# Optimization experiments

Hardware: AMD Instinct MI355X
Metric: run time of the kernel (lower is better)

The kernel has to match this reference:

```python
import jax, jax.numpy as jnp
import numpy as np

B, D, M, NKEYS = 2048, 128, 256, 32768
EST_CONST = np.float32(np.sqrt(np.pi / 2.0) / M)  # sqrt(pi/2)/projection_dim


def setup_inputs() -> dict:
    key = jax.random.key(0)
    k1, k2, k3, k4 = jax.random.split(key, 4)
    query = jax.random.normal(k1, (B, D), dtype=jnp.float32)
    # cached keys are sign-quantized JL sketches (+/-1), as produced by quantize_keys
    cached_keys = jnp.sign(jax.random.normal(k2, (NKEYS, M), dtype=jnp.float32))
    # norms of the original keys: positive, realistic magnitude ~ sqrt(D)
    key_norms = jax.random.uniform(k3, (NKEYS,), dtype=jnp.float32, minval=0.5, maxval=1.5) * np.float32(np.sqrt(D))
    sketch_matrix = jax.random.normal(k4, (M, D), dtype=jnp.float32)
    return {"query": query, "cached_keys": cached_keys, "key_norms": key_norms, "sketch_matrix": sketch_matrix}


def reference(query, cached_keys, key_norms, sketch_matrix):
    # projected_query: [B, M]
    projected_query = jnp.einsum('bd,md->bm', query, sketch_matrix)
    # inner products with quantized keys: [B, NKEYS]
    inner_products = jnp.einsum('bm,nm->bn', projected_query, cached_keys)
    estimated_scores = EST_CONST * key_norms * inner_products  # broadcast over n_keys
    return jax.nn.softmax(estimated_scores, axis=-1)
```

## Files before the change

kernel.cpp:

```cpp
#include <hip/hip_runtime.h>


#define NB 2048
#define DD 128
#define MM 256
#define NK 32768
#define EST_CONST 4.8957583489668673e-03f

typedef _Float16 half8 __attribute__((ext_vector_type(8)));
typedef _Float16 half4v __attribute__((ext_vector_type(4)));
typedef float floatx4 __attribute__((ext_vector_type(4)));

__device__ __forceinline__ void async16(const void* g, void* l) {
    __builtin_amdgcn_global_load_lds(
        (const __attribute__((address_space(1))) unsigned int*)g,
        (__attribute__((address_space(3))) unsigned int*)l,
        16, 0, 0);
}

__global__ void proj_kernel(const float* __restrict__ query,
                            const float* __restrict__ sketch,
                            _Float16* __restrict__ proj) {
    __shared__ float q[DD];
    const int b = blockIdx.x;
    const int t = threadIdx.x;
    if (t < DD) q[t] = query[b * DD + t];
    __syncthreads();
    const float* srow = sketch + t * DD;
    float acc = 0.f;
#pragma unroll
    for (int d = 0; d < DD; d += 4) {
        float4 s4 = *(const float4*)(srow + d);
        acc += s4.x * q[d] + s4.y * q[d + 1] + s4.z * q[d + 2] + s4.w * q[d + 3];
    }
    proj[b * MM + t] = (_Float16)acc;
}

__global__ void cvt_keys(const float* __restrict__ keys, _Float16* __restrict__ kh) {
    const int i = blockIdx.x * 256 + threadIdx.x;
    float4 v = ((const float4*)keys)[i];
    half4v h;
    h.x = (_Float16)v.x; h.y = (_Float16)v.y; h.z = (_Float16)v.z; h.w = (_Float16)v.w;
    ((half4v*)kh)[i] = h;
}

__global__ __launch_bounds__(256, 3)
void score_kernel(const _Float16* __restrict__ proj,
                  const _Float16* __restrict__ kh,
                  const float* __restrict__ key_norms,
                  _Float16* __restrict__ scores,
                  float* __restrict__ stats_max,
                  float* __restrict__ stats_sum) {
    __shared__ __align__(16) _Float16 sQ[128 * 64];
    __shared__ __align__(16) _Float16 sK[128 * 64];
    __shared__ float red[128][2];
    __shared__ float redS[128][2];

    const int tid  = threadIdx.x;
    const int lane = tid & 63;
    const int wave = tid >> 6;
    const int quad = lane >> 4;
    const int lc   = lane & 15;
    const int wb   = wave >> 1;
    const int wn   = wave & 1;
    const int rowBase = blockIdx.x * 128;
    const int cb      = blockIdx.y;
    const int colBase = cb * 128;

    floatx4 acc[4][4];
#pragma unroll
    for (int i = 0; i < 4; i++)
#pragma unroll
        for (int j = 0; j < 4; j++) acc[i][j] = (floatx4){0.f, 0.f, 0.f, 0.f};

    const _Float16* gQ[4];
    const _Float16* gK[4];
    int ldsOff[4];
#pragma unroll
    for (int p = 0; p < 4; p++) {
        const int c = p * 256 + tid;
        const int row = c >> 3;
        const int seg = (c & 7) ^ (row & 7);
        gQ[p] = proj + (rowBase + row) * MM + seg * 8;
        gK[p] = kh + (colBase + row) * MM + seg * 8;
        ldsOff[p] = c * 8;
    }

    for (int k0 = 0; k0 < MM; k0 += 64) {
        __syncthreads();
#pragma unroll
        for (int p = 0; p < 4; p++) {
            async16(gQ[p] + k0, &sQ[ldsOff[p]]);
            async16(gK[p] + k0, &sK[ldsOff[p]]);
        }
        __syncthreads();
#pragma unroll
        for (int kk = 0; kk < 2; kk++) {
            const int segSel = ((kk * 4 + quad) ^ (lc & 7)) * 8;
            half8 kf[4], qf[4];
#pragma unroll
            for (int s = 0; s < 4; s++) {
                kf[s] = *(const half8*)&sK[(wn * 64 + s * 16 + lc) * 64 + segSel];
                qf[s] = *(const half8*)&sQ[(wb * 64 + s * 16 + lc) * 64 + segSel];
            }
#pragma unroll
            for (int ib = 0; ib < 4; ib++)
#pragma unroll
                for (int in = 0; in < 4; in++)
                    acc[ib][in] = __builtin_amdgcn_mfma_f32_16x16x32_f16(
                        kf[in], qf[ib], acc[ib][in], 0, 0, 0);
        }
    }

#pragma unroll
    for (int in = 0; in < 4; in++) {
        const float4 nrm = *(const float4*)&key_norms[colBase + wn * 64 + in * 16 + quad * 4];
#pragma unroll
        for (int ib = 0; ib < 4; ib++) {
            acc[ib][in][0] *= EST_CONST * nrm.x;
            acc[ib][in][1] *= EST_CONST * nrm.y;
            acc[ib][in][2] *= EST_CONST * nrm.z;
            acc[ib][in][3] *= EST_CONST * nrm.w;
        }
    }

    float mcb[4];
#pragma unroll
    for (int ib = 0; ib < 4; ib++) {
        float mx = -1e30f;
#pragma unroll
        for (int in = 0; in < 4; in++)
#pragma unroll
            for (int r = 0; r < 4; r++) mx = fmaxf(mx, acc[ib][in][r]);
        mx = fmaxf(mx, __shfl_xor(mx, 16, 64));
        mx = fmaxf(mx, __shfl_xor(mx, 32, 64));
        if (quad == 0) red[wb * 64 + ib * 16 + lc][wn] = mx;
    }
    __syncthreads();
#pragma unroll
    for (int ib = 0; ib < 4; ib++) {
        const int rl = wb * 64 + ib * 16 + lc;
        mcb[ib] = fmaxf(red[rl][0], red[rl][1]);
    }
#pragma unroll
    for (int ib = 0; ib < 4; ib++) {
        float sm = 0.f;
#pragma unroll
        for (int in = 0; in < 4; in++)
#pragma unroll
            for (int r = 0; r < 4; r++) {
                const float e = __expf(acc[ib][in][r] - mcb[ib]);
                acc[ib][in][r] = e;
                sm += e;
            }
        sm += __shfl_xor(sm, 16, 64);
        sm += __shfl_xor(sm, 32, 64);
        if (quad == 0) redS[wb * 64 + ib * 16 + lc][wn] = sm;
    }
#pragma unroll
    for (int ib = 0; ib < 4; ib++) {
        const size_t rowOff = (size_t)(rowBase + wb * 64 + ib * 16 + lc) * NK;
#pragma unroll
        for (int in = 0; in < 4; in++) {
            half4v h;
            h.x = (_Float16)acc[ib][in][0];
            h.y = (_Float16)acc[ib][in][1];
            h.z = (_Float16)acc[ib][in][2];
            h.w = (_Float16)acc[ib][in][3];
            *(half4v*)&scores[rowOff + colBase + wn * 64 + in * 16 + quad * 4] = h;
        }
    }
    __syncthreads();
    if (wn == 0 && quad == 0) {
#pragma unroll
        for (int ib = 0; ib < 4; ib++) {
            const int rl = wb * 64 + ib * 16 + lc;
            const int grow = rowBase + rl;
            stats_max[grow * 256 + cb] = mcb[ib];
            stats_sum[grow * 256 + cb] = redS[rl][0] + redS[rl][1];
        }
    }
}

__global__ void combine_stats(const float* __restrict__ smax, const float* __restrict__ ssum,
                              float* __restrict__ rowM, float* __restrict__ rowR) {
    const int lane = threadIdx.x & 63;
    const int row = blockIdx.x * 4 + (threadIdx.x >> 6);
    const float4 mv = ((const float4*)(smax + row * 256))[lane];
    float m = fmaxf(fmaxf(mv.x, mv.y), fmaxf(mv.z, mv.w));
#pragma unroll
    for (int d = 1; d < 64; d <<= 1) m = fmaxf(m, __shfl_xor(m, d, 64));
    const float4 sv = ((const float4*)(ssum + row * 256))[lane];
    float l = sv.x * __expf(mv.x - m) + sv.y * __expf(mv.y - m) +
              sv.z * __expf(mv.z - m) + sv.w * __expf(mv.w - m);
#pragma unroll
    for (int d = 1; d < 64; d <<= 1) l += __shfl_xor(l, d, 64);
    if (lane == 0) {
        rowM[row] = m;
        rowR[row] = 1.0f / l;
    }
}

__global__ __launch_bounds__(256)
void norm_kernel(const _Float16* __restrict__ scores,
                 const float* __restrict__ smax,
                 const float* __restrict__ rowM, const float* __restrict__ rowR,
                 float* __restrict__ out) {
    const int idx = blockIdx.x * 256 + threadIdx.x;
    const int row = idx >> 12;
    const int c8 = (idx & 4095) << 3;
    const float scale = __expf(smax[row * 256 + (c8 >> 7)] - rowM[row]) * rowR[row];
    const half8 s = *(const half8*)(scores + ((size_t)row << 15) + c8);
    float4 o0, o1;
    o0.x = (float)s[0] * scale; o0.y = (float)s[1] * scale;
    o0.z = (float)s[2] * scale; o0.w = (float)s[3] * scale;
    o1.x = (float)s[4] * scale; o1.y = (float)s[5] * scale;
    o1.z = (float)s[6] * scale; o1.w = (float)s[7] * scale;
    float4* op = (float4*)(out + ((size_t)row << 15) + c8);
    op[0] = o0;
    op[1] = o1;
}

extern "C" void kernel_launch(void* const* d_in, const int* in_sizes, int n_in,
                              void* d_out, int out_size, void* d_ws, size_t ws_size,
                              hipStream_t stream) {
    const float* query  = (const float*)d_in[0];
    const float* keys   = (const float*)d_in[1];
    const float* norms  = (const float*)d_in[2];
    const float* sketch = (const float*)d_in[3];
    float* out = (float*)d_out;

    char* ws = (char*)d_ws;
    const size_t MB = 1024 * 1024;
    _Float16* kh     = (_Float16*)(ws);
    _Float16* proj   = (_Float16*)(ws + 16 * MB);
    _Float16* scores = (_Float16*)(ws + 17 * MB);
    float* smax      = (float*)(ws + 145 * MB);
    float* ssum      = (float*)(ws + 147 * MB);
    float* rowM      = (float*)(ws + 149 * MB);
    float* rowR      = (float*)(ws + 149 * MB + 8192);

    hipLaunchKernelGGL(proj_kernel, dim3(NB), dim3(256), 0, stream, query, sketch, proj);
    hipLaunchKernelGGL(cvt_keys, dim3(NK * MM / 4 / 256), dim3(256), 0, stream, keys, kh);
    hipLaunchKernelGGL(score_kernel, dim3(NB / 128, NK / 128), dim3(256), 0, stream,
                       proj, kh, norms, scores, smax, ssum);
    hipLaunchKernelGGL(combine_stats, dim3(NB / 4), dim3(256), 0, stream,
                       smax, ssum, rowM, rowR);
    hipLaunchKernelGGL(norm_kernel, dim3((NB * NK / 8) / 256), dim3(256), 0, stream,
                       scores, smax, rowM, rowR, out);
}
```

Baseline: 436.3 us.

## Stage score tiles through LDS for coalesced stores and precompute block scales

The score kernel now writes its exp tiles into a padded shared-memory buffer that reuses the Q/K staging space. It then emits full 128-column rows with 16-byte coalesced stores, replacing the scattered 8-byte stores. The grid is transposed so that consecutive blocks walk key columns. combine_stats now precomputes a per-row, per-column-block scale, so norm_kernel does one lookup instead of an exp, and norm_kernel uses 4-wide nontemporal stores. Costs are an extra LDS round trip and barrier, plus more threads in norm_kernel.

```diff
diff --git a/kernel.cpp b/kernel.cpp
--- a/kernel.cpp
+++ b/kernel.cpp
@@ -51,10 +51,11 @@
                   _Float16* __restrict__ scores,
                   float* __restrict__ stats_max,
                   float* __restrict__ stats_sum) {
-    __shared__ __align__(16) _Float16 sQ[128 * 64];
-    __shared__ __align__(16) _Float16 sK[128 * 64];
+    __shared__ __align__(16) _Float16 smem[17408];
     __shared__ float red[128][2];
     __shared__ float redS[128][2];
+    _Float16* sQ = smem;
+    _Float16* sK = smem + 8192;
 
     const int tid  = threadIdx.x;
     const int lane = tid & 63;
@@ -63,9 +64,9 @@
     const int lc   = lane & 15;
     const int wb   = wave >> 1;
     const int wn   = wave & 1;
-    const int rowBase = blockIdx.x * 128;
-    const int cb      = blockIdx.y;
+    const int cb      = blockIdx.x;
     const int colBase = cb * 128;
+    const int rowBase = blockIdx.y * 128;
 
     floatx4 acc[4][4];
 #pragma unroll
@@ -124,7 +125,6 @@
         }
     }
 
-    float mcb[4];
 #pragma unroll
     for (int ib = 0; ib < 4; ib++) {
         float mx = -1e30f;
@@ -137,6 +137,7 @@
         if (quad == 0) red[wb * 64 + ib * 16 + lc][wn] = mx;
     }
     __syncthreads();
+    float mcb[4];
 #pragma unroll
     for (int ib = 0; ib < 4; ib++) {
         const int rl = wb * 64 + ib * 16 + lc;
@@ -146,29 +147,19 @@
     for (int ib = 0; ib < 4; ib++) {
         float sm = 0.f;
 #pragma unroll
-        for (int in = 0; in < 4; in++)
+        for (int in = 0; in < 4; in++) {
+            half4v h;
 #pragma unroll
             for (int r = 0; r < 4; r++) {
                 const float e = __expf(acc[ib][in][r] - mcb[ib]);
-                acc[ib][in][r] = e;
+                h[r] = (_Float16)e;
                 sm += e;
             }
+            *(half4v*)&smem[(wb * 64 + ib * 16 + lc) * 136 + wn * 64 + in * 16 + quad * 4] = h;
+        }
         sm += __shfl_xor(sm, 16, 64);
         sm += __shfl_xor(sm, 32, 64);
         if (quad == 0) redS[wb * 64 + ib * 16 + lc][wn] = sm;
-    }
-#pragma unroll
-    for (int ib = 0; ib < 4; ib++) {
-        const size_t rowOff = (size_t)(rowBase + wb * 64 + ib * 16 + lc) * NK;
-#pragma unroll
-        for (int in = 0; in < 4; in++) {
-            half4v h;
-            h.x = (_Float16)acc[ib][in][0];
-            h.y = (_Float16)acc[ib][in][1];
-            h.z = (_Float16)acc[ib][in][2];
-            h.w = (_Float16)acc[ib][in][3];
-            *(half4v*)&scores[rowOff + colBase + wn * 64 + in * 16 + quad * 4] = h;
-        }
     }
     __syncthreads();
     if (wn == 0 && quad == 0) {
@@ -180,10 +171,18 @@
             stats_sum[grow * 256 + cb] = redS[rl][0] + redS[rl][1];
         }
     }
+#pragma unroll
+    for (int p = 0; p < 8; p++) {
+        const int flat = p * 2048 + tid * 8;
+        const int row = flat >> 7;
+        const int col = flat & 127;
+        half8 v = *(const half8*)&smem[row * 136 + col];
+        *(half8*)&scores[(size_t)(rowBase + row) * NK + colBase + col] = v;
+    }
 }
 
 __global__ void combine_stats(const float* __restrict__ smax, const float* __restrict__ ssum,
-                              float* __restrict__ rowM, float* __restrict__ rowR) {
+                              float* __restrict__ cbscale) {
     const int lane = threadIdx.x & 63;
     const int row = blockIdx.x * 4 + (threadIdx.x >> 6);
     const float4 mv = ((const float4*)(smax + row * 256))[lane];
@@ -195,30 +194,30 @@
               sv.z * __expf(mv.z - m) + sv.w * __expf(mv.w - m);
 #pragma unroll
     for (int d = 1; d < 64; d <<= 1) l += __shfl_xor(l, d, 64);
-    if (lane == 0) {
-        rowM[row] = m;
-        rowR[row] = 1.0f / l;
-    }
+    const float rL = 1.0f / l;
+    float4 sc;
+    sc.x = __expf(mv.x - m) * rL;
+    sc.y = __expf(mv.y - m) * rL;
+    sc.z = __expf(mv.z - m) * rL;
+    sc.w = __expf(mv.w - m) * rL;
+    ((float4*)(cbscale + row * 256))[lane] = sc;
 }
 
 __global__ __launch_bounds__(256)
 void norm_kernel(const _Float16* __restrict__ scores,
-                 const float* __restrict__ smax,
-                 const float* __restrict__ rowM, const float* __restrict__ rowR,
+                 const float* __restrict__ cbscale,
                  float* __restrict__ out) {
-    const int idx = blockIdx.x * 256 + threadIdx.x;
-    const int row = idx >> 12;
-    const int c8 = (idx & 4095) << 3;
-    const float scale = __expf(smax[row * 256 + (c8 >> 7)] - rowM[row]) * rowR[row];
-    const half8 s = *(const half8*)(scores + ((size_t)row << 15) + c8);
-    float4 o0, o1;
-    o0.x = (float)s[0] * scale; o0.y = (float)s[1] * scale;
-    o0.z = (float)s[2] * scale; o0.w = (float)s[3] * scale;
-    o1.x = (float)s[4] * scale; o1.y = (float)s[5] * scale;
-    o1.z = (float)s[6] * scale; o1.w = (float)s[7] * scale;
-    float4* op = (float4*)(out + ((size_t)row << 15) + c8);
-    op[0] = o0;
-    op[1] = o1;
+    const unsigned idx = blockIdx.x * 256 + threadIdx.x;
+    const int row = idx >> 13;
+    const int c4 = (idx & 8191) << 2;
+    const float scale = cbscale[row * 256 + (c4 >> 7)];
+    const half4v s = *(const half4v*)(scores + ((size_t)row << 15) + c4);
+    floatx4 o;
+    o[0] = (float)s.x * scale;
+    o[1] = (float)s.y * scale;
+    o[2] = (float)s.z * scale;
+    o[3] = (float)s.w * scale;
+    __builtin_nontemporal_store(o, (floatx4*)(out + ((size_t)row << 15) + c4));
 }
 
 extern "C" void kernel_launch(void* const* d_in, const int* in_sizes, int n_in,
@@ -237,15 +236,14 @@
     _Float16* scores = (_Float16*)(ws + 17 * MB);
     float* smax      = (float*)(ws + 145 * MB);
     float* ssum      = (float*)(ws + 147 * MB);
-    float* rowM      = (float*)(ws + 149 * MB);
-    float* rowR      = (float*)(ws + 149 * MB + 8192);
+    float* cbscale   = (float*)(ws + 149 * MB);
 
     hipLaunchKernelGGL(proj_kernel, dim3(NB), dim3(256), 0, stream, query, sketch, proj);
     hipLaunchKernelGGL(cvt_keys, dim3(NK * MM / 4 / 256), dim3(256), 0, stream, keys, kh);
-    hipLaunchKernelGGL(score_kernel, dim3(NB / 128, NK / 128), dim3(256), 0, stream,
+    hipLaunchKernelGGL(score_kernel, dim3(NK / 128, NB / 128), dim3(256), 0, stream,
                        proj, kh, norms, scores, smax, ssum);
     hipLaunchKernelGGL(combine_stats, dim3(NB / 4), dim3(256), 0, stream,
-                       smax, ssum, rowM, rowR);
-    hipLaunchKernelGGL(norm_kernel, dim3((NB * NK / 8) / 256), dim3(256), 0, stream,
-                       scores, smax, rowM, rowR, out);
-}
+                       smax, ssum, cbscale);
+    hipLaunchKernelGGL(norm_kernel, dim3((NB * NK / 4) / 256), dim3(256), 0, stream,
+                       scores, cbscale, out);
+}
```

After: 403.4 us. -7.6%, faster.
